# Optimization experiments

Hardware: AMD Instinct MI355X
Metric: run time of the kernel (lower is better)

The kernel has to match this reference:

```python
import jax, jax.numpy as jnp
import numpy as np

K = 128      # knowledge_n
E = 4096     # exer_n
S = 2048     # student_n
M = 512      # number of supervised exercises (ex_id)
NUM_UPDATE = 3
THRESHOLD = 0.05
H = 1.0


def setup_inputs() -> dict:
    key = jax.random.key(0)
    ks = jax.random.split(key, 16)
    U_embeding = jax.random.uniform(ks[0], (S, K), dtype=jnp.float32)
    W = jax.random.uniform(ks[1], (K, E), dtype=jnp.float32)
    beiTa_1 = jax.random.uniform(ks[2], (K, E), dtype=jnp.float32)
    beiTa_2 = jax.random.uniform(ks[3], (E, 1), dtype=jnp.float32)
    B = jax.random.uniform(ks[4], (K, E, K), dtype=jnp.float32)
    guess_slip = jax.random.normal(ks[5], (E, 2), dtype=jnp.float32)
    A_emb = jax.random.normal(ks[6], (E, 3), dtype=jnp.float32)
    gamma_c = jax.random.normal(ks[7], (E, 1), dtype=jnp.float32)
    gamma_e = jax.random.normal(ks[8], (E, 1), dtype=jnp.float32)
    alpha = jax.random.normal(ks[9], (E, 1), dtype=jnp.float32)
    score = jax.random.randint(ks[10], (E, 1), 0, 2).astype(jnp.float32)
    user_k_kc = (jax.random.uniform(ks[11], (K, E)) < 0.3).astype(jnp.float32)
    # multi-hot question->concept map, ~4 concepts per exercise, at least 1
    q_kn = (jax.random.uniform(ks[12], (E, K)) < 4.0 / K).astype(jnp.float32)
    q_kn = q_kn.at[jnp.arange(E), jax.random.randint(ks[13], (E,), 0, K)].set(1.0)
    d = q_kn.sum(axis=1, keepdims=True)  # exercise degree, >= 1
    ex_id = jax.random.randint(ks[14], (M,), 0, E, dtype=jnp.int32)
    kn_id = jnp.arange(K, dtype=jnp.int32)
    stu_id = 7
    return dict(U_embeding=U_embeding, W=W, beiTa_1=beiTa_1, beiTa_2=beiTa_2,
                B=B, guess_slip=guess_slip, A_emb=A_emb, gamma_c=gamma_c,
                gamma_e=gamma_e, alpha=alpha, score=score, user_k_kc=user_k_kc,
                q_kn=q_kn, d=d, stu_id=stu_id, kn_id=kn_id, ex_id=ex_id)


def reference(U_embeding, W, beiTa_1, beiTa_2, B, guess_slip, A_emb,
              gamma_c, gamma_e, alpha, score, user_k_kc, q_kn, d,
              stu_id, kn_id, ex_id):
    # The torch loop `for cur_kn in kn_id: update(cur_kn, U_update[num-1])` is a
    # Jacobi sweep: every concept update reads the PREVIOUS state, so all
    # concepts can be computed in one vectorized pass per iteration.
    Bdiag = jnp.einsum('kek->ke', B)           # B[k, e, k], (K, E)
    dvec = d[:, 0]                              # (E,)
    sc = score[:, 0]                            # (E,)
    upd = jnp.zeros((K,), dtype=bool).at[kn_id].set(True)

    def step(u):                                # u: (K,) current mastery state
        # ---- Ic (eq. 7): per-exercise interaction term ----
        su = q_kn @ u                           # (E,)  sum of mastered concepts
        yc = jnp.exp(-(sc - su / dvec) ** 2)    # (E,)
        Pc = jnp.concatenate([1.0 - guess_slip, yc[:, None]], axis=1)  # (E,3)
        Ic = jax.nn.sigmoid(-jnp.sum(A_emb * Pc, axis=1))              # (E,)
        # ---- Gkc: masked, dead-zoned neighbour influence ----
        # U_gkc entries with q_kn==0 are set to 0.5, and column cur_kn is
        # zeroed; dead-zone of 0.5 contributes 0, so it reduces to a gated
        # product with the k-diagonal term subtracted out.
        dv = jnp.where(jnp.abs(u - 0.5) > THRESHOLD, u - 0.5, 0.0)      # (K,)
        qdv = q_kn * dv                         # (E, K)
        Gsum = jnp.einsum('kej,ej->ke', B, qdv) - Bdiag * qdv.T         # (K, E)
        # NOTE: the original subtracts 0.5 twice (sigmoid(...) - 0.5 then
        # reshape(...) - 0.5); replicated faithfully.
        Gkc = jax.nn.sigmoid(-Gsum) - 1.0       # (K, E)
        # ---- Zc ----
        Zc = jax.nn.sigmoid(-(gamma_c[:, 0] / dvec) * (sc - 0.5)) - 0.5  # (E,)
        # ---- WKC and the per-concept contraction over the exercise set ----
        WK = H * Ic[None, :] * (beiTa_1 * Gkc + (beiTa_2[:, 0] * Zc)[None, :])
        s = jnp.sum(user_k_kc * W * WK, axis=1)  # ragged set via 0/1 mask, (K,)
        u_new = jax.nn.sigmoid(-s)
        return jnp.where(upd, u_new, u)

    u0 = U_embeding[stu_id]                     # (K,)
    states = [u0]
    diffs = []
    for _ in range(NUM_UPDATE):
        un = step(states[-1])
        diffs.append(jnp.linalg.norm(un - states[-1]))
        states.append(un)

    state_last = states[-1][:, None]            # U_update[-2] in torch indexing
    state_2nd_last = states[-2][:, None]        # U_update[-3]
    diff_norm = jnp.stack(diffs)

    # ---- supervised predict ----
    Ukse = (q_kn[ex_id] @ state_last) / d[ex_id] - 0.5                  # (M,1)
    predict = jax.nn.sigmoid(-(alpha[ex_id] * Ukse + gamma_e[ex_id]))   # (M,1)
    return (state_last, state_2nd_last, predict, diff_norm)
```

## Files before the change

### kernel.cpp

```cpp
#include <hip/hip_runtime.h>
#include <math.h>

#define KK 128
#define EE 4096
#define MM 512
#define CP 32

#define OFF_U    0
#define OFF_PA   128
#define OFF_PB   2176
#define OFF_CNT  4224
#define OFF_IDX  8320
#define OFF_IDXT 41088
#define OFF_PE   73856
#define OFF_GW   94336
#define OFF_HW   618624
#define OFF_BC   1142912


__global__ __launch_bounds__(256) void k_setup(
    const float* __restrict__ U, const float* __restrict__ W,
    const float* __restrict__ beiTa_1, const float* __restrict__ beiTa_2,
    const float* __restrict__ guess_slip, const float* __restrict__ A_emb,
    const float* __restrict__ gamma_c, const float* __restrict__ score,
    const float* __restrict__ ukc, const float* __restrict__ q_kn,
    const float* __restrict__ d, const int* __restrict__ stu_id,
    float* __restrict__ ws)
{
    int tid = threadIdx.x;
    int blk = blockIdx.x;
    if (blk < 16) {
        int e = blk * 256 + tid;
        int* cnt = (int*)(ws + OFF_CNT);
        signed char* idx  = (signed char*)(ws + OFF_IDX);
        signed char* idxT = (signed char*)(ws + OFF_IDXT);
        float* P01  = ws + OFF_PE;
        float* a2   = P01 + EE;
        float* scv  = a2 + EE;
        float* invd = scv + EE;
        float* bz   = invd + EE;

        int* ip32 = (int*)(idx + e * CP);
        #pragma unroll
        for (int t = 0; t < CP / 4; t++) ip32[t] = -1;
        const float4* qrow = (const float4*)(q_kn + (size_t)e * KK);
        int c = 0;
        for (int j4 = 0; j4 < KK / 4; j4++) {
            float4 q = qrow[j4];
            int j = j4 * 4;
            if (q.x > 0.5f) { if (c < CP) idx[e*CP+c] = (signed char)j;     c++; }
            if (q.y > 0.5f) { if (c < CP) idx[e*CP+c] = (signed char)(j+1); c++; }
            if (q.z > 0.5f) { if (c < CP) idx[e*CP+c] = (signed char)(j+2); c++; }
            if (q.w > 0.5f) { if (c < CP) idx[e*CP+c] = (signed char)(j+3); c++; }
        }
        c = (c < CP) ? c : CP;
        cnt[e] = c;
        for (int i = 0; i < CP; i++) idxT[(size_t)i * EE + e] = idx[e * CP + i];

        float id_ = 1.0f / d[e];
        invd[e] = id_;
        float scr = score[e];
        scv[e] = scr;
        P01[e] = A_emb[3*e] * (1.0f - guess_slip[2*e]) +
                 A_emb[3*e+1] * (1.0f - guess_slip[2*e+1]);
        a2[e] = A_emb[3*e+2];
        float zc = 1.0f / (1.0f + __expf(gamma_c[e] * id_ * (scr - 0.5f))) - 0.5f;
        bz[e] = beiTa_2[e] * zc;

        if (blk == 0 && tid < KK) ws[tid] = U[(size_t)stu_id[0] * KK + tid];
    } else {
        float* gW = ws + OFF_GW;
        float* hW = ws + OFF_HW;
        int stride = 256 * 256;
        for (int t = (blk - 16) * 256 + tid; t < KK * EE; t += stride) {
            float uw = ukc[t] * W[t];
            hW[t] = uw;
            gW[t] = uw * beiTa_1[t];
        }
    }
}

__global__ __launch_bounds__(256) void k_cp0(
    const float* __restrict__ B, float* __restrict__ ws, float* __restrict__ pout)
{
    __shared__ float lds[64 * KK];
    int tid = threadIdx.x;
    int ec = blockIdx.x;
    int k  = blockIdx.y;

    const signed char* idxT = (const signed char*)(ws + OFF_IDXT);
    float* Bc = ws + OFF_BC;

    for (int t4 = 0; t4 < 4; t4++) {
        int e0 = ec * 256 + t4 * 64;
        const float4* src = (const float4*)(B + ((size_t)k * EE + e0) * KK);
        float4* dst4 = (float4*)lds;
        #pragma unroll
        for (int it = 0; it < 8; it++)
            dst4[it * 256 + tid] = src[it * 256 + tid];
        __syncthreads();
        int eo = tid & 63;
        float* BcB = Bc + (size_t)k * CP * EE + e0 + eo;
        for (int i = tid >> 6; i < CP; i += 4) {
            int j = idxT[(size_t)i * EE + e0 + eo];
            unsigned long long m = __ballot(j >= 0);
            if (!m) break;
            if (j >= 0) BcB[(size_t)i * EE] = lds[eo * KK + j];
        }
        __syncthreads();
    }

    float* lu   = lds;
    float* sdv  = lds + 128;
    float* wred = lds + 256;
    if (tid < KK) {
        float uv = ws[tid];
        lu[tid] = uv;
        float t = uv - 0.5f;
        sdv[tid] = (fabsf(t) > 0.05f) ? t : 0.0f;
    }
    __syncthreads();

    const int* cnt = (const int*)(ws + OFF_CNT);
    const float* P01  = ws + OFF_PE;
    const float* a2   = P01 + EE;
    const float* scv  = a2 + EE;
    const float* invd = scv + EE;
    const float* bzv  = invd + EE;
    const float* gW   = ws + OFF_GW;
    const float* hW   = ws + OFF_HW;

    int e = ec * 256 + tid;
    int c = cnt[e];
    const signed char* it = idxT + e;
    const float* bp = Bc + (size_t)k * CP * EE + e;
    float su = 0.0f, gs = 0.0f;
    for (int i = 0; i < c; i++) {
        int j   = it[(size_t)i * EE];
        float b = bp[(size_t)i * EE];
        su += lu[j];
        gs = fmaf(b, (j != k) ? sdv[j] : 0.0f, gs);
    }
    float t0 = scv[e] - su * invd[e];
    float yc = __expf(-t0 * t0);
    float Ic = 1.0f / (1.0f + __expf(P01[e] + a2[e] * yc));
    float Gkc = 1.0f / (1.0f + __expf(gs)) - 1.0f;
    size_t o = (size_t)k * EE + e;
    float v = Ic * (gW[o] * Gkc + hW[o] * bzv[e]);

    #pragma unroll
    for (int m = 1; m < 64; m <<= 1) v += __shfl_xor(v, m);
    if ((tid & 63) == 0) wred[tid >> 6] = v;
    __syncthreads();
    if (tid == 0) pout[k * 16 + ec] = wred[0] + wred[1] + wred[2] + wred[3];
}

__global__ __launch_bounds__(256) void k_phase(
    float* __restrict__ ws, float* __restrict__ out,
    const float* __restrict__ pin, float* __restrict__ pout, int phase)
{
    __shared__ float lu[KK];
    __shared__ float sdv[KK];
    __shared__ float red2[KK];
    __shared__ float wred[4];
    int tid = threadIdx.x;
    int ec = blockIdx.x;
    int k  = blockIdx.y;
    int e  = ec * 256 + tid;

    if (tid < KK) {
        float s = 0.0f;
        const float* p = pin + tid * 16;
        #pragma unroll
        for (int t = 0; t < 16; t++) s += p[t];
        float uv = 1.0f / (1.0f + __expf(s));
        lu[tid] = uv;
        float t = uv - 0.5f;
        sdv[tid] = (fabsf(t) > 0.05f) ? t : 0.0f;
    }
    __syncthreads();

    const int* cnt = (const int*)(ws + OFF_CNT);
    const signed char* idxT = (const signed char*)(ws + OFF_IDXT);
    const float* P01  = ws + OFF_PE;
    const float* a2   = P01 + EE;
    const float* scv  = a2 + EE;
    const float* invd = scv + EE;
    const float* bzv  = invd + EE;
    const float* gW   = ws + OFF_GW;
    const float* hW   = ws + OFF_HW;
    const float* Bc   = ws + OFF_BC;

    int c = cnt[e];
    const signed char* it = idxT + e;
    const float* bp = Bc + (size_t)k * CP * EE + e;
    float su = 0.0f, gs = 0.0f;
    for (int i = 0; i < c; i++) {
        int j   = it[(size_t)i * EE];
        float b = bp[(size_t)i * EE];
        su += lu[j];
        gs = fmaf(b, (j != k) ? sdv[j] : 0.0f, gs);
    }
    float t0 = scv[e] - su * invd[e];
    float yc = __expf(-t0 * t0);
    float Ic = 1.0f / (1.0f + __expf(P01[e] + a2[e] * yc));
    float Gkc = 1.0f / (1.0f + __expf(gs)) - 1.0f;
    size_t o = (size_t)k * EE + e;
    float v = Ic * (gW[o] * Gkc + hW[o] * bzv[e]);

    #pragma unroll
    for (int m = 1; m < 64; m <<= 1) v += __shfl_xor(v, m);
    if ((tid & 63) == 0) wred[tid >> 6] = v;
    __syncthreads();
    if (tid == 0) pout[k * 16 + ec] = wred[0] + wred[1] + wred[2] + wred[3];

    if (blockIdx.x == 0 && blockIdx.y == 0) {
        if (tid < KK) {
            float dd = lu[tid] - ws[tid];
            red2[tid] = dd * dd;
        }
        __syncthreads();
        for (int s2 = 64; s2 > 0; s2 >>= 1) {
            if (tid < s2) red2[tid] += red2[tid + s2];
            __syncthreads();
        }
        if (tid == 0) out[768 + (phase - 1)] = sqrtf(red2[0]);
        if (tid < KK) {
            ws[tid] = lu[tid];
            if (phase == 2) out[128 + tid] = lu[tid];
        }
    }
}

__global__ __launch_bounds__(512) void k_final(
    float* __restrict__ ws, float* __restrict__ out, const float* __restrict__ pin,
    const int* __restrict__ ex_id, const float* __restrict__ alpha,
    const float* __restrict__ gamma_e)
{
    __shared__ float un_s[KK];
    __shared__ float red[KK];
    int tid = threadIdx.x;
    if (tid < KK) {
        float s = 0.0f;
        const float* p = pin + tid * 16;
        #pragma unroll
        for (int t = 0; t < 16; t++) s += p[t];
        float un = 1.0f / (1.0f + __expf(s));
        float dd = un - ws[tid];
        red[tid] = dd * dd;
        un_s[tid] = un;
        out[tid] = un;
    }
    __syncthreads();
    for (int s2 = 64; s2 > 0; s2 >>= 1) {
        if (tid < s2) red[tid] += red[tid + s2];
        __syncthreads();
    }
    if (tid == 0) out[770] = sqrtf(red[0]);

    const int* cnt = (const int*)(ws + OFF_CNT);
    const signed char* idx = (const signed char*)(ws + OFF_IDX);
    const float* invd = ws + OFF_PE + 3 * EE;
    int e = ex_id[tid];
    int c = cnt[e];
    const signed char* ip = idx + (size_t)e * CP;
    float su = 0.0f;
    for (int i = 0; i < c; i++) su += un_s[ip[i]];
    float Ukse = su * invd[e] - 0.5f;
    out[256 + tid] = 1.0f / (1.0f + __expf(alpha[e] * Ukse + gamma_e[e]));
}

extern "C" void kernel_launch(void* const* d_in, const int* in_sizes, int n_in,
                              void* d_out, int out_size, void* d_ws, size_t ws_size,
                              hipStream_t stream) {
    const float* U          = (const float*)d_in[0];
    const float* W          = (const float*)d_in[1];
    const float* beiTa_1    = (const float*)d_in[2];
    const float* beiTa_2    = (const float*)d_in[3];
    const float* B          = (const float*)d_in[4];
    const float* guess_slip = (const float*)d_in[5];
    const float* A_emb      = (const float*)d_in[6];
    const float* gamma_c    = (const float*)d_in[7];
    const float* gamma_e    = (const float*)d_in[8];
    const float* alpha      = (const float*)d_in[9];
    const float* score      = (const float*)d_in[10];
    const float* ukc        = (const float*)d_in[11];
    const float* q_kn       = (const float*)d_in[12];
    const float* d          = (const float*)d_in[13];
    const int*   stu_id     = (const int*)d_in[14];
    const int*   ex_id      = (const int*)d_in[16];
    float* out = (float*)d_out;
    float* ws  = (float*)d_ws;
    float* pA = ws + OFF_PA;
    float* pB = ws + OFF_PB;

    k_setup<<<272, 256, 0, stream>>>(U, W, beiTa_1, beiTa_2, guess_slip, A_emb,
                                     gamma_c, score, ukc, q_kn, d, stu_id, ws);
    k_cp0<<<dim3(16, 128), 256, 0, stream>>>(B, ws, pA);
    k_phase<<<dim3(16, 128), 256, 0, stream>>>(ws, out, pA, pB, 1);
    k_phase<<<dim3(16, 128), 256, 0, stream>>>(ws, out, pB, pA, 2);
    k_final<<<1, 512, 0, stream>>>(ws, out, pA, ex_id, alpha, gamma_e);
}
```

Baseline: 457.0 us.

## Fuse setup into first sweep kernel and recompute W products on the fly

Removes the separate setup kernel by having each block of the first sweep build its own per-exercise concept index list in shared memory and compute per-exercise scalars locally, with only k==0 blocks writing them to workspace. The precomputed gW/hW arrays are dropped, and every phase instead reads ukc, W and beiTa_1 directly and multiplies them. This removes one launch and the write and reread of two large intermediate arrays, but each of the 2048 blocks now re-scans q_kn rows redundantly, and the phase kernels read three arrays instead of two. k_final now reads the transposed index layout.

```diff
diff --git a/kernel.cpp b/kernel.cpp
--- a/kernel.cpp
+++ b/kernel.cpp
@@ -10,87 +10,61 @@
 #define OFF_PA   128
 #define OFF_PB   2176
 #define OFF_CNT  4224
-#define OFF_IDX  8320
 #define OFF_IDXT 41088
 #define OFF_PE   73856
-#define OFF_GW   94336
-#define OFF_HW   618624
 #define OFF_BC   1142912
 
 
-__global__ __launch_bounds__(256) void k_setup(
-    const float* __restrict__ U, const float* __restrict__ W,
-    const float* __restrict__ beiTa_1, const float* __restrict__ beiTa_2,
-    const float* __restrict__ guess_slip, const float* __restrict__ A_emb,
-    const float* __restrict__ gamma_c, const float* __restrict__ score,
-    const float* __restrict__ ukc, const float* __restrict__ q_kn,
-    const float* __restrict__ d, const int* __restrict__ stu_id,
-    float* __restrict__ ws)
-{
-    int tid = threadIdx.x;
-    int blk = blockIdx.x;
-    if (blk < 16) {
-        int e = blk * 256 + tid;
-        int* cnt = (int*)(ws + OFF_CNT);
-        signed char* idx  = (signed char*)(ws + OFF_IDX);
-        signed char* idxT = (signed char*)(ws + OFF_IDXT);
-        float* P01  = ws + OFF_PE;
-        float* a2   = P01 + EE;
-        float* scv  = a2 + EE;
-        float* invd = scv + EE;
-        float* bz   = invd + EE;
-
-        int* ip32 = (int*)(idx + e * CP);
-        #pragma unroll
-        for (int t = 0; t < CP / 4; t++) ip32[t] = -1;
-        const float4* qrow = (const float4*)(q_kn + (size_t)e * KK);
-        int c = 0;
-        for (int j4 = 0; j4 < KK / 4; j4++) {
-            float4 q = qrow[j4];
-            int j = j4 * 4;
-            if (q.x > 0.5f) { if (c < CP) idx[e*CP+c] = (signed char)j;     c++; }
-            if (q.y > 0.5f) { if (c < CP) idx[e*CP+c] = (signed char)(j+1); c++; }
-            if (q.z > 0.5f) { if (c < CP) idx[e*CP+c] = (signed char)(j+2); c++; }
-            if (q.w > 0.5f) { if (c < CP) idx[e*CP+c] = (signed char)(j+3); c++; }
-        }
-        c = (c < CP) ? c : CP;
-        cnt[e] = c;
-        for (int i = 0; i < CP; i++) idxT[(size_t)i * EE + e] = idx[e * CP + i];
-
-        float id_ = 1.0f / d[e];
-        invd[e] = id_;
-        float scr = score[e];
-        scv[e] = scr;
-        P01[e] = A_emb[3*e] * (1.0f - guess_slip[2*e]) +
-                 A_emb[3*e+1] * (1.0f - guess_slip[2*e+1]);
-        a2[e] = A_emb[3*e+2];
-        float zc = 1.0f / (1.0f + __expf(gamma_c[e] * id_ * (scr - 0.5f))) - 0.5f;
-        bz[e] = beiTa_2[e] * zc;
-
-        if (blk == 0 && tid < KK) ws[tid] = U[(size_t)stu_id[0] * KK + tid];
-    } else {
-        float* gW = ws + OFF_GW;
-        float* hW = ws + OFF_HW;
-        int stride = 256 * 256;
-        for (int t = (blk - 16) * 256 + tid; t < KK * EE; t += stride) {
-            float uw = ukc[t] * W[t];
-            hW[t] = uw;
-            gW[t] = uw * beiTa_1[t];
-        }
-    }
-}
-
-__global__ __launch_bounds__(256) void k_cp0(
-    const float* __restrict__ B, float* __restrict__ ws, float* __restrict__ pout)
+__global__ __launch_bounds__(256) void k_fused0(
+    const float* __restrict__ B, const float* __restrict__ U,
+    const float* __restrict__ W, const float* __restrict__ beiTa_1,
+    const float* __restrict__ beiTa_2, const float* __restrict__ guess_slip,
+    const float* __restrict__ A_emb, const float* __restrict__ gamma_c,
+    const float* __restrict__ score, const float* __restrict__ ukc,
+    const float* __restrict__ q_kn, const float* __restrict__ d,
+    const int* __restrict__ stu_id, float* __restrict__ ws,
+    float* __restrict__ pout)
 {
     __shared__ float lds[64 * KK];
+    __shared__ signed char lidxT[CP][256];
     int tid = threadIdx.x;
     int ec = blockIdx.x;
     int k  = blockIdx.y;
-
-    const signed char* idxT = (const signed char*)(ws + OFF_IDXT);
+    int e  = ec * 256 + tid;
+
+    #pragma unroll
+    for (int i = 0; i < CP; i++) lidxT[i][tid] = -1;
+    const float4* qrow = (const float4*)(q_kn + (size_t)e * KK);
+    int c = 0;
+    for (int j4 = 0; j4 < KK / 4; j4++) {
+        float4 q = qrow[j4];
+        int j = j4 * 4;
+        if (q.x > 0.5f) { if (c < CP) lidxT[c][tid] = (signed char)j;     c++; }
+        if (q.y > 0.5f) { if (c < CP) lidxT[c][tid] = (signed char)(j+1); c++; }
+        if (q.z > 0.5f) { if (c < CP) lidxT[c][tid] = (signed char)(j+2); c++; }
+        if (q.w > 0.5f) { if (c < CP) lidxT[c][tid] = (signed char)(j+3); c++; }
+    }
+    c = (c < CP) ? c : CP;
+
+    float id_ = 1.0f / d[e];
+    float scr = score[e];
+    float p01 = A_emb[3*e] * (1.0f - guess_slip[2*e]) +
+                A_emb[3*e+1] * (1.0f - guess_slip[2*e+1]);
+    float a2v = A_emb[3*e+2];
+    float zc  = 1.0f / (1.0f + __expf(gamma_c[e] * id_ * (scr - 0.5f))) - 0.5f;
+    float bzr = beiTa_2[e] * zc;
+
+    if (k == 0) {
+        ((int*)(ws + OFF_CNT))[e] = c;
+        signed char* idxT = (signed char*)(ws + OFF_IDXT);
+        for (int i = 0; i < CP; i++) idxT[(size_t)i * EE + e] = lidxT[i][tid];
+        float* pe = ws + OFF_PE;
+        pe[e] = p01; pe[EE + e] = a2v; pe[2*EE + e] = scr;
+        pe[3*EE + e] = id_; pe[4*EE + e] = bzr;
+    }
+    __syncthreads();
+
     float* Bc = ws + OFF_BC;
-
     for (int t4 = 0; t4 < 4; t4++) {
         int e0 = ec * 256 + t4 * 64;
         const float4* src = (const float4*)(B + ((size_t)k * EE + e0) * KK);
@@ -100,9 +74,10 @@
             dst4[it * 256 + tid] = src[it * 256 + tid];
         __syncthreads();
         int eo = tid & 63;
+        int el = t4 * 64 + eo;
         float* BcB = Bc + (size_t)k * CP * EE + e0 + eo;
         for (int i = tid >> 6; i < CP; i += 4) {
-            int j = idxT[(size_t)i * EE + e0 + eo];
+            int j = lidxT[i][el];
             unsigned long long m = __ballot(j >= 0);
             if (!m) break;
             if (j >= 0) BcB[(size_t)i * EE] = lds[eo * KK + j];
@@ -114,23 +89,74 @@
     float* sdv  = lds + 128;
     float* wred = lds + 256;
     if (tid < KK) {
-        float uv = ws[tid];
+        float uv = U[(size_t)stu_id[0] * KK + tid];
         lu[tid] = uv;
         float t = uv - 0.5f;
         sdv[tid] = (fabsf(t) > 0.05f) ? t : 0.0f;
+        if (ec == 0 && k == 0) ws[tid] = uv;
+    }
+    __syncthreads();
+
+    const float* bp = Bc + (size_t)k * CP * EE + e;
+    float su = 0.0f, gs = 0.0f;
+    for (int i = 0; i < c; i++) {
+        int j   = lidxT[i][tid];
+        float b = bp[(size_t)i * EE];
+        su += lu[j];
+        gs = fmaf(b, (j != k) ? sdv[j] : 0.0f, gs);
+    }
+    float t0 = scr - su * id_;
+    float yc = __expf(-t0 * t0);
+    float Ic = 1.0f / (1.0f + __expf(p01 + a2v * yc));
+    float Gkc = 1.0f / (1.0f + __expf(gs)) - 1.0f;
+    size_t o = (size_t)k * EE + e;
+    float uw = ukc[o] * W[o];
+    float g  = uw * beiTa_1[o];
+    float v  = Ic * (g * Gkc + uw * bzr);
+
+    #pragma unroll
+    for (int m = 1; m < 64; m <<= 1) v += __shfl_xor(v, m);
+    if ((tid & 63) == 0) wred[tid >> 6] = v;
+    __syncthreads();
+    if (tid == 0) pout[k * 16 + ec] = wred[0] + wred[1] + wred[2] + wred[3];
+}
+
+__global__ __launch_bounds__(256) void k_phase(
+    float* __restrict__ ws, float* __restrict__ out,
+    const float* __restrict__ pin, float* __restrict__ pout,
+    const float* __restrict__ ukc, const float* __restrict__ W,
+    const float* __restrict__ beiTa_1, int phase)
+{
+    __shared__ float lu[KK];
+    __shared__ float sdv[KK];
+    __shared__ float red2[KK];
+    __shared__ float wred[4];
+    int tid = threadIdx.x;
+    int ec = blockIdx.x;
+    int k  = blockIdx.y;
+    int e  = ec * 256 + tid;
+
+    if (tid < KK) {
+        float s = 0.0f;
+        const float* p = pin + tid * 16;
+        #pragma unroll
+        for (int t = 0; t < 16; t++) s += p[t];
+        float uv = 1.0f / (1.0f + __expf(s));
+        lu[tid] = uv;
+        float t = uv - 0.5f;
+        sdv[tid] = (fabsf(t) > 0.05f) ? t : 0.0f;
     }
     __syncthreads();
 
     const int* cnt = (const int*)(ws + OFF_CNT);
+    const signed char* idxT = (const signed char*)(ws + OFF_IDXT);
     const float* P01  = ws + OFF_PE;
     const float* a2   = P01 + EE;
     const float* scv  = a2 + EE;
     const float* invd = scv + EE;
     const float* bzv  = invd + EE;
-    const float* gW   = ws + OFF_GW;
-    const float* hW   = ws + OFF_HW;
-
-    int e = ec * 256 + tid;
+    const float* Bc   = ws + OFF_BC;
+
     int c = cnt[e];
     const signed char* it = idxT + e;
     const float* bp = Bc + (size_t)k * CP * EE + e;
@@ -146,67 +172,9 @@
     float Ic = 1.0f / (1.0f + __expf(P01[e] + a2[e] * yc));
     float Gkc = 1.0f / (1.0f + __expf(gs)) - 1.0f;
     size_t o = (size_t)k * EE + e;
-    float v = Ic * (gW[o] * Gkc + hW[o] * bzv[e]);
-
-    #pragma unroll
-    for (int m = 1; m < 64; m <<= 1) v += __shfl_xor(v, m);
-    if ((tid & 63) == 0) wred[tid >> 6] = v;
-    __syncthreads();
-    if (tid == 0) pout[k * 16 + ec] = wred[0] + wred[1] + wred[2] + wred[3];
-}
-
-__global__ __launch_bounds__(256) void k_phase(
-    float* __restrict__ ws, float* __restrict__ out,
-    const float* __restrict__ pin, float* __restrict__ pout, int phase)
-{
-    __shared__ float lu[KK];
-    __shared__ float sdv[KK];
-    __shared__ float red2[KK];
-    __shared__ float wred[4];
-    int tid = threadIdx.x;
-    int ec = blockIdx.x;
-    int k  = blockIdx.y;
-    int e  = ec * 256 + tid;
-
-    if (tid < KK) {
-        float s = 0.0f;
-        const float* p = pin + tid * 16;
-        #pragma unroll
-        for (int t = 0; t < 16; t++) s += p[t];
-        float uv = 1.0f / (1.0f + __expf(s));
-        lu[tid] = uv;
-        float t = uv - 0.5f;
-        sdv[tid] = (fabsf(t) > 0.05f) ? t : 0.0f;
-    }
-    __syncthreads();
-
-    const int* cnt = (const int*)(ws + OFF_CNT);
-    const signed char* idxT = (const signed char*)(ws + OFF_IDXT);
-    const float* P01  = ws + OFF_PE;
-    const float* a2   = P01 + EE;
-    const float* scv  = a2 + EE;
-    const float* invd = scv + EE;
-    const float* bzv  = invd + EE;
-    const float* gW   = ws + OFF_GW;
-    const float* hW   = ws + OFF_HW;
-    const float* Bc   = ws + OFF_BC;
-
-    int c = cnt[e];
-    const signed char* it = idxT + e;
-    const float* bp = Bc + (size_t)k * CP * EE + e;
-    float su = 0.0f, gs = 0.0f;
-    for (int i = 0; i < c; i++) {
-        int j   = it[(size_t)i * EE];
-        float b = bp[(size_t)i * EE];
-        su += lu[j];
-        gs = fmaf(b, (j != k) ? sdv[j] : 0.0f, gs);
-    }
-    float t0 = scv[e] - su * invd[e];
-    float yc = __expf(-t0 * t0);
-    float Ic = 1.0f / (1.0f + __expf(P01[e] + a2[e] * yc));
-    float Gkc = 1.0f / (1.0f + __expf(gs)) - 1.0f;
-    size_t o = (size_t)k * EE + e;
-    float v = Ic * (gW[o] * Gkc + hW[o] * bzv[e]);
+    float uw = ukc[o] * W[o];
+    float g  = uw * beiTa_1[o];
+    float v  = Ic * (g * Gkc + uw * bzv[e]);
 
     #pragma unroll
     for (int m = 1; m < 64; m <<= 1) v += __shfl_xor(v, m);
@@ -259,13 +227,12 @@
     if (tid == 0) out[770] = sqrtf(red[0]);
 
     const int* cnt = (const int*)(ws + OFF_CNT);
-    const signed char* idx = (const signed char*)(ws + OFF_IDX);
+    const signed char* idxT = (const signed char*)(ws + OFF_IDXT);
     const float* invd = ws + OFF_PE + 3 * EE;
     int e = ex_id[tid];
     int c = cnt[e];
-    const signed char* ip = idx + (size_t)e * CP;
     float su = 0.0f;
-    for (int i = 0; i < c; i++) su += un_s[ip[i]];
+    for (int i = 0; i < c; i++) su += un_s[idxT[(size_t)i * EE + e]];
     float Ukse = su * invd[e] - 0.5f;
     out[256 + tid] = 1.0f / (1.0f + __expf(alpha[e] * Ukse + gamma_e[e]));
 }
@@ -294,10 +261,10 @@
     float* pA = ws + OFF_PA;
     float* pB = ws + OFF_PB;
 
-    k_setup<<<272, 256, 0, stream>>>(U, W, beiTa_1, beiTa_2, guess_slip, A_emb,
-                                     gamma_c, score, ukc, q_kn, d, stu_id, ws);
-    k_cp0<<<dim3(16, 128), 256, 0, stream>>>(B, ws, pA);
-    k_phase<<<dim3(16, 128), 256, 0, stream>>>(ws, out, pA, pB, 1);
-    k_phase<<<dim3(16, 128), 256, 0, stream>>>(ws, out, pB, pA, 2);
+    k_fused0<<<dim3(16, 128), 256, 0, stream>>>(B, U, W, beiTa_1, beiTa_2,
+                                                guess_slip, A_emb, gamma_c, score,
+                                                ukc, q_kn, d, stu_id, ws, pA);
+    k_phase<<<dim3(16, 128), 256, 0, stream>>>(ws, out, pA, pB, ukc, W, beiTa_1, 1);
+    k_phase<<<dim3(16, 128), 256, 0, stream>>>(ws, out, pB, pA, ukc, W, beiTa_1, 2);
     k_final<<<1, 512, 0, stream>>>(ws, out, pA, ex_id, alpha, gamma_e);
 }
```

After: 463.5 us. About the same (+1.4%).

## Gather B entries directly per thread instead of staging full rows in LDS

Applied to the files above, without the earlier changes.

The first phase kernel no longer streams every full 128-float row of B through shared memory. Each thread now reads only the few B[k,e,j] entries its exercise needs, straight from global memory, and writes the compacted copy in the same loop. This avoids reading the whole 256 MB B tensor, at the cost of scattered, uncoalesced 4-byte reads across rows 512 bytes apart. The setup kernel's weight-precompute grid is also halved.

```diff
diff --git a/kernel.cpp b/kernel.cpp
--- a/kernel.cpp
+++ b/kernel.cpp
@@ -71,7 +71,7 @@
     } else {
         float* gW = ws + OFF_GW;
         float* hW = ws + OFF_HW;
-        int stride = 256 * 256;
+        int stride = 128 * 256;
         for (int t = (blk - 16) * 256 + tid; t < KK * EE; t += stride) {
             float uw = ukc[t] * W[t];
             hW[t] = uw;
@@ -80,39 +80,17 @@
     }
 }
 
-__global__ __launch_bounds__(256) void k_cp0(
+__global__ __launch_bounds__(256) void k_phase0(
     const float* __restrict__ B, float* __restrict__ ws, float* __restrict__ pout)
 {
-    __shared__ float lds[64 * KK];
+    __shared__ float lu[KK];
+    __shared__ float sdv[KK];
+    __shared__ float wred[4];
     int tid = threadIdx.x;
     int ec = blockIdx.x;
     int k  = blockIdx.y;
-
-    const signed char* idxT = (const signed char*)(ws + OFF_IDXT);
-    float* Bc = ws + OFF_BC;
-
-    for (int t4 = 0; t4 < 4; t4++) {
-        int e0 = ec * 256 + t4 * 64;
-        const float4* src = (const float4*)(B + ((size_t)k * EE + e0) * KK);
-        float4* dst4 = (float4*)lds;
-        #pragma unroll
-        for (int it = 0; it < 8; it++)
-            dst4[it * 256 + tid] = src[it * 256 + tid];
-        __syncthreads();
-        int eo = tid & 63;
-        float* BcB = Bc + (size_t)k * CP * EE + e0 + eo;
-        for (int i = tid >> 6; i < CP; i += 4) {
-            int j = idxT[(size_t)i * EE + e0 + eo];
-            unsigned long long m = __ballot(j >= 0);
-            if (!m) break;
-            if (j >= 0) BcB[(size_t)i * EE] = lds[eo * KK + j];
-        }
-        __syncthreads();
-    }
-
-    float* lu   = lds;
-    float* sdv  = lds + 128;
-    float* wred = lds + 256;
+    int e  = ec * 256 + tid;
+
     if (tid < KK) {
         float uv = ws[tid];
         lu[tid] = uv;
@@ -122,6 +100,7 @@
     __syncthreads();
 
     const int* cnt = (const int*)(ws + OFF_CNT);
+    const signed char* idxT = (const signed char*)(ws + OFF_IDXT);
     const float* P01  = ws + OFF_PE;
     const float* a2   = P01 + EE;
     const float* scv  = a2 + EE;
@@ -129,15 +108,17 @@
     const float* bzv  = invd + EE;
     const float* gW   = ws + OFF_GW;
     const float* hW   = ws + OFF_HW;
-
-    int e = ec * 256 + tid;
+    float* Bc = ws + OFF_BC;
+
     int c = cnt[e];
     const signed char* it = idxT + e;
-    const float* bp = Bc + (size_t)k * CP * EE + e;
+    const float* Brow = B + ((size_t)k * EE + e) * KK;
+    float* BcB = Bc + (size_t)k * CP * EE + e;
     float su = 0.0f, gs = 0.0f;
     for (int i = 0; i < c; i++) {
         int j   = it[(size_t)i * EE];
-        float b = bp[(size_t)i * EE];
+        float b = Brow[j];
+        BcB[(size_t)i * EE] = b;
         su += lu[j];
         gs = fmaf(b, (j != k) ? sdv[j] : 0.0f, gs);
     }
@@ -294,9 +275,9 @@
     float* pA = ws + OFF_PA;
     float* pB = ws + OFF_PB;
 
-    k_setup<<<272, 256, 0, stream>>>(U, W, beiTa_1, beiTa_2, guess_slip, A_emb,
+    k_setup<<<144, 256, 0, stream>>>(U, W, beiTa_1, beiTa_2, guess_slip, A_emb,
                                      gamma_c, score, ukc, q_kn, d, stu_id, ws);
-    k_cp0<<<dim3(16, 128), 256, 0, stream>>>(B, ws, pA);
+    k_phase0<<<dim3(16, 128), 256, 0, stream>>>(B, ws, pA);
     k_phase<<<dim3(16, 128), 256, 0, stream>>>(ws, out, pA, pB, 1);
     k_phase<<<dim3(16, 128), 256, 0, stream>>>(ws, out, pB, pA, 2);
     k_final<<<1, 512, 0, stream>>>(ws, out, pA, ex_id, alpha, gamma_e);
```

New measurement: 433.0 us. -5.3%, faster.
